# Optimization experiments

Hardware: AMD Instinct MI355X
Metric: run time of the kernel (lower is better)

## Reference

```python
import jax, jax.numpy as jnp
import numpy as np

N_NODES = 50000
N_EDGES = 800000
NODE_FEAT = 3
HID = 64
L = 4


def setup_inputs() -> dict:
    key = jax.random.key(0)
    ks = jax.random.split(key, 16)
    s = 0.05  # init scale
    inp = {
        'node_pos': jax.random.normal(ks[0], (N_NODES, 3), jnp.float32),
        'node_features': jax.random.normal(ks[1], (N_NODES, NODE_FEAT), jnp.float32),
        'edge_index': jax.random.randint(ks[2], (2, N_EDGES), 0, N_NODES, jnp.int64),
        # encoders
        'enc_w': jax.random.normal(ks[3], (NODE_FEAT, HID), jnp.float32) * s,
        'enc_b': jnp.zeros((HID,), jnp.float32),
        'edge_enc_w': jax.random.normal(ks[4], (3, HID), jnp.float32) * s,
        'edge_enc_b': jnp.zeros((HID,), jnp.float32),
        # stacked per-layer GNOLayer params
        'ew1': jax.random.normal(ks[5], (L, 3 * HID, HID), jnp.float32) * s,
        'eb1': jnp.zeros((L, HID), jnp.float32),
        'ew2': jax.random.normal(ks[6], (L, HID, HID), jnp.float32) * s,
        'eb2': jnp.zeros((L, HID), jnp.float32),
        'nw1': jax.random.normal(ks[7], (L, 2 * HID, HID), jnp.float32) * s,
        'nb1': jnp.zeros((L, HID), jnp.float32),
        'nw2': jax.random.normal(ks[8], (L, HID, HID), jnp.float32) * s,
        'nb2': jnp.zeros((L, HID), jnp.float32),
        # decoder
        'dec_w': jax.random.normal(ks[9], (HID, 1), jnp.float32) * s,
        'dec_b': jnp.zeros((1,), jnp.float32),
    }
    return inp


def reference(node_pos, node_features, edge_index, enc_w, enc_b, edge_enc_w,
              edge_enc_b, ew1, eb1, ew2, eb2, nw1, nb1, nw2, nb2, dec_w, dec_b):
    src, dst = edge_index[0], edge_index[1]
    edge_vec = node_pos[dst] - node_pos[src]            # [E, 3]
    h = node_features @ enc_w + enc_b                   # [N, H]
    e = edge_vec @ edge_enc_w + edge_enc_b              # [E, H]

    def layer(h, p):
        w1, b1, w2, b2, m1, c1, m2, c2 = p
        edge_in = jnp.concatenate([h[src], h[dst], e], axis=-1)   # [E, 3H]
        msg = jax.nn.relu(edge_in @ w1 + b1) @ w2 + b2            # [E, H]
        agg = jax.ops.segment_sum(msg, dst, num_segments=N_NODES)  # [N, H]
        node_in = jnp.concatenate([h, agg], axis=-1)              # [N, 2H]
        return jax.nn.relu(node_in @ m1 + c1) @ m2 + c2, None

    h, _ = jax.lax.scan(layer, h, (ew1, eb1, ew2, eb2, nw1, nb1, nw2, nb2))
    return h @ dec_w + dec_b                            # [N, 1]
```

## Files before the change

kernel.cpp:

```cpp
#include <hip/hip_runtime.h>

#define N_NODES 50000
#define N_EDGES 800000
#define HID 64
#define LAYERS 4
#define EP_CAP 2048
#define SCAN_NBLK 25

typedef unsigned short u16;
typedef __attribute__((ext_vector_type(8))) __bf16 bf16x8;
typedef __attribute__((ext_vector_type(8))) unsigned short u16x8;
typedef __attribute__((ext_vector_type(4))) float f32x4;
typedef _Float16 f16x2 __attribute__((ext_vector_type(2)));

__device__ __forceinline__ u16 f2bf(float f) {
  unsigned u = __builtin_bit_cast(unsigned, f);
  u += 0x7fffu + ((u >> 16) & 1u);
  return (u16)(u >> 16);
}
__device__ __forceinline__ float bf2f(u16 s) {
  return __builtin_bit_cast(float, ((unsigned)s) << 16);
}
__device__ __forceinline__ u16 f2h(float f) {
  return __builtin_bit_cast(u16, (_Float16)f);
}
__device__ __forceinline__ unsigned pkadd(unsigned a, unsigned b) {
  f16x2 r = __builtin_bit_cast(f16x2, a) + __builtin_bit_cast(f16x2, b);
  return __builtin_bit_cast(unsigned, r);
}
__device__ __forceinline__ unsigned pkmax0(unsigned x) {
  unsigned r, z = 0u;
  asm("v_pk_max_f16 %0, %1, %2" : "=v"(r) : "v"(x), "v"(z));
  return r;
}

__global__ __launch_bounds__(256) void init_kernel(
    const float* __restrict__ ew1, const float* __restrict__ eb1,
    const float* __restrict__ ew2, const float* __restrict__ eb2,
    const float* __restrict__ nw1, const float* __restrict__ nw2,
    const float* __restrict__ edge_enc_w, const float* __restrict__ edge_enc_b,
    u16* W1abT, float* Wvx, float* b1x,
    u16* NB1T, float* bb2, u16* M2T, int* __restrict__ cnt) {
  const int T = gridDim.x * 256;
  int tid = blockIdx.x * 256 + threadIdx.x;
  for (int i = tid; i < N_NODES; i += T) cnt[i] = 0;
  const int szA = LAYERS * 128 * 64, szV = LAYERS * 3 * 64, szB = LAYERS * 64;
  const int szN = LAYERS * 64 * 128, szb2 = LAYERS * 64, szM = LAYERS * 64 * 64;
  const int tot = szA + szV + szB + szN + szb2 + szM;
  for (int i = tid; i < tot; i += T) {
    int idx = i;
    if (idx < szA) {
      int l = idx / (128 * 64); int r = idx % (128 * 64);
      int nfc = r / 64; int k = r % 64;
      int half = nfc >> 6, f = nfc & 63;
      W1abT[idx] = f2bf(ew1[(l * 192 + half * 64 + k) * 64 + f]);
      continue;
    }
    idx -= szA;
    if (idx < szV) {
      int l = idx / 192, r = idx % 192, a = r / 64, f = r % 64;
      float s = 0.f;
      for (int m = 0; m < 64; ++m) s += edge_enc_w[a * 64 + m] * ew1[(l * 192 + 128 + m) * 64 + f];
      Wvx[idx] = s;
      continue;
    }
    idx -= szV;
    if (idx < szB) {
      int l = idx / 64, f = idx % 64;
      float s = eb1[l * 64 + f];
      for (int m = 0; m < 64; ++m) s += edge_enc_b[m] * ew1[(l * 192 + 128 + m) * 64 + f];
      b1x[idx] = s;
      continue;
    }
    idx -= szB;
    if (idx < szN) {
      int l = idx / 8192, r = idx % 8192, f = r / 128, k = r % 128;
      float v;
      if (k < 64) v = nw1[(l * 128 + k) * 64 + f];
      else {
        int j = k - 64; float s = 0.f;
        for (int g = 0; g < 64; ++g)
          s += ew2[(l * 64 + j) * 64 + g] * nw1[(l * 128 + 64 + g) * 64 + f];
        v = s;
      }
      NB1T[idx] = f2bf(v);
      continue;
    }
    idx -= szN;
    if (idx < szb2) {
      int l = idx / 64, f = idx % 64;
      float s = 0.f;
      for (int g = 0; g < 64; ++g) s += eb2[l * 64 + g] * nw1[(l * 128 + 64 + g) * 64 + f];
      bb2[idx] = s;
      continue;
    }
    idx -= szb2;
    int l = idx / 4096, r = idx % 4096, f = r / 64, k = r % 64;
    M2T[idx] = f2bf(nw2[(l * 64 + k) * 64 + f]);
  }
}

__global__ __launch_bounds__(256) void hist_kernel(const int* __restrict__ dstA,
                                                   int* __restrict__ cnt,
                                                   int* __restrict__ rank) {
  int idx = blockIdx.x * 256 + threadIdx.x;
  if (idx < N_EDGES) rank[idx] = atomicAdd(&cnt[dstA[idx]], 1);
}

__global__ __launch_bounds__(256) void scan1_kernel(const int* __restrict__ cnt,
                                                    int* __restrict__ offs,
                                                    int* __restrict__ partials) {
  __shared__ int sm[2048];
  __shared__ int ws2[256];
  int t = threadIdx.x, b = blockIdx.x;
  int base = b * 2048;
#pragma unroll
  for (int i = 0; i < 8; ++i) {
    int idx = base + i * 256 + t;
    sm[i * 256 + t] = (idx < N_NODES) ? cnt[idx] : 0;
  }
  __syncthreads();
  int loc[8]; int s = 0;
#pragma unroll
  for (int i = 0; i < 8; ++i) { loc[i] = s; s += sm[t * 8 + i]; }
  ws2[t] = s;
  __syncthreads();
  for (int off = 1; off < 256; off <<= 1) {
    int u = (t >= off) ? ws2[t - off] : 0;
    __syncthreads();
    ws2[t] += u;
    __syncthreads();
  }
  int tbase = (t > 0) ? ws2[t - 1] : 0;
  if (t == 255) partials[b] = ws2[255];
#pragma unroll
  for (int i = 0; i < 8; ++i) {
    int idx = base + t * 8 + i;
    if (idx < N_NODES) offs[idx] = tbase + loc[i];
  }
}

__global__ __launch_bounds__(256) void scan3_kernel(int* __restrict__ offs,
                                                    const int* __restrict__ partials) {
  __shared__ int pref;
  int blk = (blockIdx.x * 256) >> 11;
  if (threadIdx.x == 0) {
    int s = 0;
    for (int i = 0; i < blk; ++i) s += partials[i];
    pref = s;
  }
  __syncthreads();
  int idx = blockIdx.x * 256 + threadIdx.x;
  if (idx < N_NODES) offs[idx] += pref;
}

__global__ __launch_bounds__(256) void scatter_kernel(const int* __restrict__ ei,
                                                      const int* __restrict__ offs,
                                                      const int* __restrict__ rank,
                                                      int* __restrict__ srcB) {
  int idx = blockIdx.x * 256 + threadIdx.x;
  if (idx >= N_EDGES) return;
  int s = ei[idx], d = ei[N_EDGES + idx];
  srcB[offs[d] + rank[idx]] = s << 7;
}

__global__ __launch_bounds__(256) void encsu_kernel(
    const float* __restrict__ nf, const float* __restrict__ enc_w,
    const float* __restrict__ enc_b,
    const u16* __restrict__ W1abT, const float* __restrict__ Wvx,
    const float* __restrict__ b1x, const float* __restrict__ pos,
    u16* __restrict__ h, u16* __restrict__ Sarr, u16* __restrict__ Uarr) {
  __shared__ u16 hT[64 * 72];
  __shared__ float sPos[192];
  __shared__ float sNf[192];
  int t = threadIdx.x;
  int lane = t & 63, wvi = t >> 6;
  int n16 = lane & 15, quad = lane >> 4;
  int n0 = blockIdx.x * 64;
  if (t < 192) {
    int idx = n0 * 3 + t;
    bool ok = idx < N_NODES * 3;
    sPos[t] = ok ? pos[idx] : 0.f;
    sNf[t] = ok ? nf[idx] : 0.f;
  }
  __syncthreads();
  {
    int n = t >> 2, g = t & 3;
    float x0 = sNf[n * 3], x1 = sNf[n * 3 + 1], x2 = sNf[n * 3 + 2];
    u16x8 v0, v1;
#pragma unroll
    for (int j = 0; j < 8; ++j) {
      int jj = g * 16 + j;
      v0[j] = f2bf(enc_b[jj] + x0 * enc_w[jj] + x1 * enc_w[64 + jj] + x2 * enc_w[128 + jj]);
      int jj2 = jj + 8;
      v1[j] = f2bf(enc_b[jj2] + x0 * enc_w[jj2] + x1 * enc_w[64 + jj2] + x2 * enc_w[128 + jj2]);
    }
    *(u16x8*)(hT + n * 72 + g * 16) = v0;
    *(u16x8*)(hT + n * 72 + g * 16 + 8) = v1;
    int gn = n0 + n;
    if (gn < N_NODES) {
      *(u16x8*)(h + (size_t)gn * 64 + g * 16) = v0;
      *(u16x8*)(h + (size_t)gn * 64 + g * 16 + 8) = v1;
    }
  }
  __syncthreads();

  bf16x8 B[2][2];
  float w0[2], w1[2], w2[2], bb[2]; bool isU[2];
#pragma unroll
  for (int nt = 0; nt < 2; ++nt) {
    int col = wvi * 32 + nt * 16 + n16;
    const u16* p = W1abT + (size_t)col * 64 + quad * 8;
    B[nt][0] = __builtin_bit_cast(bf16x8, *(const u16x8*)(p));
    B[nt][1] = __builtin_bit_cast(bf16x8, *(const u16x8*)(p + 32));
    int f = col & 63; isU[nt] = col >= 64;
    w0[nt] = Wvx[f];
    w1[nt] = Wvx[64 + f];
    w2[nt] = Wvx[128 + f];
    bb[nt] = b1x[f];
  }
  f32x4 acc[4][2];
#pragma unroll
  for (int m = 0; m < 4; ++m)
#pragma unroll
    for (int nt = 0; nt < 2; ++nt) acc[m][nt] = (f32x4){0.f, 0.f, 0.f, 0.f};
#pragma unroll
  for (int m = 0; m < 4; ++m) {
    const u16* hp = hT + (m * 16 + n16) * 72 + quad * 8;
    bf16x8 a0 = __builtin_bit_cast(bf16x8, *(const u16x8*)(hp));
    bf16x8 a1 = __builtin_bit_cast(bf16x8, *(const u16x8*)(hp + 32));
#pragma unroll
    for (int nt = 0; nt < 2; ++nt) {
      acc[m][nt] = __builtin_amdgcn_mfma_f32_16x16x32_bf16(a0, B[nt][0], acc[m][nt], 0, 0, 0);
      acc[m][nt] = __builtin_amdgcn_mfma_f32_16x16x32_bf16(a1, B[nt][1], acc[m][nt], 0, 0, 0);
    }
  }
#pragma unroll
  for (int m = 0; m < 4; ++m)
#pragma unroll
    for (int nt = 0; nt < 2; ++nt) {
      int col = wvi * 32 + nt * 16 + n16;
      int f = col & 63;
#pragma unroll
      for (int r = 0; r < 4; ++r) {
        int e = m * 16 + quad * 4 + r;
        int grow = n0 + e;
        if (grow < N_NODES) {
          float P = sPos[e * 3] * w0[nt] + sPos[e * 3 + 1] * w1[nt] + sPos[e * 3 + 2] * w2[nt];
          if (!isU[nt]) Sarr[(size_t)grow * 64 + f] = f2h(acc[m][nt][r] - P);
          else          Uarr[(size_t)grow * 64 + f] = f2h(acc[m][nt][r] + P + bb[nt]);
        }
      }
    }
}

__global__ __launch_bounds__(256) void layer_kernel(
    const u16* __restrict__ h, const int* __restrict__ srcB,
    const int* __restrict__ offs,
    const u16* __restrict__ Sr, const u16* __restrict__ Ur,
    const u16* __restrict__ NB1T, const float* __restrict__ nb1,
    const float* __restrict__ bb2,
    const u16* __restrict__ M2T, const float* __restrict__ nb2,
    u16* __restrict__ hnext, int layer,
    const u16* __restrict__ W1abT, const float* __restrict__ Wvx,
    const float* __restrict__ b1x, const float* __restrict__ pos,
    u16* __restrict__ Sw, u16* __restrict__ Uw,
    const float* __restrict__ dec_w, const float* __restrict__ dec_b,
    float* __restrict__ out) {
  __shared__ int sIdx[EP_CAP];
  __shared__ int sOff[33];
  __shared__ u16 aggT[32 * 72];
  __shared__ u16 Hs[32 * 72];
  __shared__ float sPos[96];
  __shared__ float sRed[32][8];
  int t = threadIdx.x;
  int lane = t & 63, wvi = t >> 6;
  int n16 = lane & 15, quad = lane >> 4;
  int F = wvi * 16;
  int n0 = blockIdx.x * 32;

  if (t <= 32) {
    int d = n0 + t;
    sOff[t] = (d < N_NODES) ? offs[d] : N_EDGES;
  }
  if (t >= 64 && t < 160) {
    int i = t - 64;
    int idx = n0 * 3 + i;
    sPos[i] = (idx < N_NODES * 3) ? pos[idx] : 0.f;
  }
  __syncthreads();
  int eS = sOff[0];
  int nE = sOff[32] - eS;
  bool fit = (nE <= EP_CAP);
  if (fit) {
    for (int i = t; i < nE; i += 256) sIdx[i] = srcB[eS + i];
    if (t == 0 && nE < EP_CAP) sIdx[nE] = 0;
  }
  __syncthreads();

  {
    int c = lane & 31, half = lane >> 5;
    unsigned cbu = (unsigned)(c << 2);
    const char* __restrict__ Sb = (const char*)Sr;
    const char* __restrict__ Ub = (const char*)Ur;
    for (int i = 0; i < 8; i += 2) {
      int lnA = wvi * 8 + i;
      int dA = n0 + lnA;
      int e0A = sOff[lnA], degA = sOff[lnA + 1] - e0A;
      int e0B = sOff[lnA + 1], degB = sOff[lnA + 2] - e0B;
      int dAc = dA < N_NODES ? dA : N_NODES - 1;
      int dBc = (dA + 1) < N_NODES ? (dA + 1) : N_NODES - 1;
      unsigned upA = *(const unsigned*)(Ub + (size_t)dAc * 128 + cbu);
      unsigned upB = *(const unsigned*)(Ub + (size_t)dBc * 128 + cbu);
      float saA = 0.f, sbA = 0.f, saB = 0.f, sbB = 0.f;
      int relA = (degA > 0) ? (e0A - eS) : 0;
      int relB = (degB > 0) ? (e0B - eS) : 0;
      int g0A = (degA > 0) ? e0A : 0;
      int g0B = (degB > 0) ? e0B : 0;
      int degMin = degA < degB ? degA : degB;
      int degMax = degA > degB ? degA : degB;
      int fullr = degMin >> 4;
      int rmax = (degMax + 15) >> 4;
      if (fit) {
        int r = 0;
        for (; r < fullr; ++r) {
          int base = r * 16 + half;
          unsigned wA[8], wB[8];
#pragma unroll
          for (int kk = 0; kk < 8; ++kk) {
            int j = base + 2 * kk;
            wA[kk] = *(const unsigned*)(Sb + (unsigned)sIdx[relA + j] + cbu);
            wB[kk] = *(const unsigned*)(Sb + (unsigned)sIdx[relB + j] + cbu);
          }
          unsigned pA = 0u, pB = 0u;
#pragma unroll
          for (int kk = 0; kk < 8; ++kk) {
            pA = pkadd(pA, pkmax0(pkadd(wA[kk], upA)));
            pB = pkadd(pB, pkmax0(pkadd(wB[kk], upB)));
          }
          f16x2 hA2 = __builtin_bit_cast(f16x2, pA);
          f16x2 hB2 = __builtin_bit_cast(f16x2, pB);
          saA += (float)hA2[0]; sbA += (float)hA2[1];
          saB += (float)hB2[0]; sbB += (float)hB2[1];
        }
        for (; r < rmax; ++r) {
          int base = r * 16 + half;
          unsigned wA[8], wB[8]; bool okA[8], okB[8];
#pragma unroll
          for (int kk = 0; kk < 8; ++kk) {
            int j = base + 2 * kk;
            okA[kk] = j < degA;
            wA[kk] = *(const unsigned*)(Sb + (unsigned)sIdx[relA + (okA[kk] ? j : 0)] + cbu);
            okB[kk] = j < degB;
            wB[kk] = *(const unsigned*)(Sb + (unsigned)sIdx[relB + (okB[kk] ? j : 0)] + cbu);
          }
          unsigned pA = 0u, pB = 0u;
#pragma unroll
          for (int kk = 0; kk < 8; ++kk) {
            unsigned zA = pkmax0(pkadd(wA[kk], upA));
            pA = pkadd(pA, okA[kk] ? zA : 0u);
            unsigned zB = pkmax0(pkadd(wB[kk], upB));
            pB = pkadd(pB, okB[kk] ? zB : 0u);
          }
          f16x2 hA2 = __builtin_bit_cast(f16x2, pA);
          f16x2 hB2 = __builtin_bit_cast(f16x2, pB);
          saA += (float)hA2[0]; sbA += (float)hA2[1];
          saB += (float)hB2[0]; sbB += (float)hB2[1];
        }
      } else {
        for (int r = 0; r < rmax; ++r) {
          int base = r * 16 + half;
          unsigned wA[8], wB[8]; bool okA[8], okB[8];
#pragma unroll
          for (int kk = 0; kk < 8; ++kk) {
            int j = base + 2 * kk;
            okA[kk] = j < degA;
            wA[kk] = *(const unsigned*)(Sb + (unsigned)srcB[g0A + (okA[kk] ? j : 0)] + cbu);
            okB[kk] = j < degB;
            wB[kk] = *(const unsigned*)(Sb + (unsigned)srcB[g0B + (okB[kk] ? j : 0)] + cbu);
          }
          unsigned pA = 0u, pB = 0u;
#pragma unroll
          for (int kk = 0; kk < 8; ++kk) {
            unsigned zA = pkmax0(pkadd(wA[kk], upA));
            pA = pkadd(pA, okA[kk] ? zA : 0u);
            unsigned zB = pkmax0(pkadd(wB[kk], upB));
            pB = pkadd(pB, okB[kk] ? zB : 0u);
          }
          f16x2 hA2 = __builtin_bit_cast(f16x2, pA);
          f16x2 hB2 = __builtin_bit_cast(f16x2, pB);
          saA += (float)hA2[0]; sbA += (float)hA2[1];
          saB += (float)hB2[0]; sbB += (float)hB2[1];
        }
      }
      saA += __shfl_xor(saA, 32);  sbA += __shfl_xor(sbA, 32);
      saB += __shfl_xor(saB, 32);  sbB += __shfl_xor(sbB, 32);
      if (half == 0) {
        unsigned pk = (unsigned)f2bf(saA) | ((unsigned)f2bf(sbA) << 16);
        *(unsigned*)((char*)aggT + (size_t)lnA * 144 + cbu) = pk;
        unsigned pk2 = (unsigned)f2bf(saB) | ((unsigned)f2bf(sbB) << 16);
        *(unsigned*)((char*)aggT + (size_t)(lnA + 1) * 144 + cbu) = pk2;
      }
    }
  }
  __syncthreads();

  bf16x8 B1[4], B2[2];
  {
    const u16* p = NB1T + (size_t)(layer * 64 + F + n16) * 128 + quad * 8;
#pragma unroll
    for (int ks = 0; ks < 4; ++ks) B1[ks] = __builtin_bit_cast(bf16x8, *(const u16x8*)(p + ks * 32));
    const u16* q = M2T + (size_t)(layer * 64 + F + n16) * 64 + quad * 8;
#pragma unroll
    for (int ks = 0; ks < 2; ++ks) B2[ks] = __builtin_bit_cast(bf16x8, *(const u16x8*)(q + ks * 32));
  }
  float bias1 = nb1[layer * 64 + F + n16];
  float bb2f = bb2[layer * 64 + F + n16];
  float bias2 = nb2[layer * 64 + F + n16];

  f32x4 acc[2];
#pragma unroll
  for (int m = 0; m < 2; ++m) acc[m] = (f32x4){0.f, 0.f, 0.f, 0.f};
#pragma unroll
  for (int m = 0; m < 2; ++m) {
    int row = n0 + m * 16 + n16;
    if (row >= N_NODES) row = N_NODES - 1;
    const u16* hp = h + (size_t)row * 64 + quad * 8;
    const u16* ap = aggT + (m * 16 + n16) * 72 + quad * 8;
    bf16x8 a0 = __builtin_bit_cast(bf16x8, *(const u16x8*)(hp));
    bf16x8 a1 = __builtin_bit_cast(bf16x8, *(const u16x8*)(hp + 32));
    bf16x8 a2 = __builtin_bit_cast(bf16x8, *(const u16x8*)(ap));
    bf16x8 a3 = __builtin_bit_cast(bf16x8, *(const u16x8*)(ap + 32));
    acc[m] = __builtin_amdgcn_mfma_f32_16x16x32_bf16(a0, B1[0], acc[m], 0, 0, 0);
    acc[m] = __builtin_amdgcn_mfma_f32_16x16x32_bf16(a1, B1[1], acc[m], 0, 0, 0);
    acc[m] = __builtin_amdgcn_mfma_f32_16x16x32_bf16(a2, B1[2], acc[m], 0, 0, 0);
    acc[m] = __builtin_amdgcn_mfma_f32_16x16x32_bf16(a3, B1[3], acc[m], 0, 0, 0);
  }
#pragma unroll
  for (int m = 0; m < 2; ++m)
#pragma unroll
    for (int r = 0; r < 4; ++r) {
      int e = m * 16 + quad * 4 + r;
      float dg = (float)(sOff[e + 1] - sOff[e]);
      float v = acc[m][r] + bias1 + dg * bb2f;
      v = v > 0.f ? v : 0.f;
      Hs[e * 72 + F + n16] = f2bf(v);
    }
  __syncthreads();

  float c2[2][4];
#pragma unroll
  for (int m = 0; m < 2; ++m) {
    const u16* hp = Hs + (m * 16 + n16) * 72 + quad * 8;
    f32x4 cc = (f32x4){0.f, 0.f, 0.f, 0.f};
#pragma unroll
    for (int ks = 0; ks < 2; ++ks) {
      bf16x8 a = __builtin_bit_cast(bf16x8, *(const u16x8*)(hp + ks * 32));
      cc = __builtin_amdgcn_mfma_f32_16x16x32_bf16(a, B2[ks], cc, 0, 0, 0);
    }
#pragma unroll
    for (int r = 0; r < 4; ++r) c2[m][r] = cc[r] + bias2;
  }
  __syncthreads();

#pragma unroll
  for (int m = 0; m < 2; ++m)
#pragma unroll
    for (int r = 0; r < 4; ++r) {
      int e = m * 16 + quad * 4 + r;
      u16 hv = f2bf(c2[m][r]);
      Hs[e * 72 + F + n16] = hv;
      int gn = n0 + e;
      if (layer < LAYERS - 1 && gn < N_NODES)
        hnext[(size_t)gn * 64 + F + n16] = hv;
    }
  __syncthreads();

  if (layer < LAYERS - 1) {
    int lp = layer + 1;
    bf16x8 B3[2][2];
    float w0[2], w1[2], w2[2], bb[2]; bool isU[2];
#pragma unroll
    for (int nt = 0; nt < 2; ++nt) {
      int col = wvi * 32 + nt * 16 + n16;
      const u16* p = W1abT + (size_t)(lp * 128 + col) * 64 + quad * 8;
      B3[nt][0] = __builtin_bit_cast(bf16x8, *(const u16x8*)(p));
      B3[nt][1] = __builtin_bit_cast(bf16x8, *(const u16x8*)(p + 32));
      int f = col & 63; isU[nt] = col >= 64;
      w0[nt] = Wvx[(lp * 3 + 0) * 64 + f];
      w1[nt] = Wvx[(lp * 3 + 1) * 64 + f];
      w2[nt] = Wvx[(lp * 3 + 2) * 64 + f];
      bb[nt] = b1x[lp * 64 + f];
    }
    f32x4 a3[2][2];
#pragma unroll
    for (int m = 0; m < 2; ++m)
#pragma unroll
      for (int nt = 0; nt < 2; ++nt) a3[m][nt] = (f32x4){0.f, 0.f, 0.f, 0.f};
#pragma unroll
    for (int m = 0; m < 2; ++m) {
      const u16* hp = Hs + (m * 16 + n16) * 72 + quad * 8;
      bf16x8 a0 = __builtin_bit_cast(bf16x8, *(const u16x8*)(hp));
      bf16x8 a1 = __builtin_bit_cast(bf16x8, *(const u16x8*)(hp + 32));
#pragma unroll
      for (int nt = 0; nt < 2; ++nt) {
        a3[m][nt] = __builtin_amdgcn_mfma_f32_16x16x32_bf16(a0, B3[nt][0], a3[m][nt], 0, 0, 0);
        a3[m][nt] = __builtin_amdgcn_mfma_f32_16x16x32_bf16(a1, B3[nt][1], a3[m][nt], 0, 0, 0);
      }
    }
#pragma unroll
    for (int m = 0; m < 2; ++m)
#pragma unroll
      for (int nt = 0; nt < 2; ++nt) {
        int col = wvi * 32 + nt * 16 + n16;
        int f = col & 63;
#pragma unroll
        for (int r = 0; r < 4; ++r) {
          int e = m * 16 + quad * 4 + r;
          int grow = n0 + e;
          if (grow < N_NODES) {
            float P = sPos[e * 3] * w0[nt] + sPos[e * 3 + 1] * w1[nt] + sPos[e * 3 + 2] * w2[nt];
            if (!isU[nt]) Sw[(size_t)grow * 64 + f] = f2h(a3[m][nt][r] - P);
            else          Uw[(size_t)grow * 64 + f] = f2h(a3[m][nt][r] + P + bb[nt]);
          }
        }
      }
  } else {
    int e = t >> 3, part = t & 7;
    float s = 0.f;
#pragma unroll
    for (int j = 0; j < 8; ++j)
      s += bf2f(Hs[e * 72 + part * 8 + j]) * dec_w[part * 8 + j];
    sRed[e][part] = s;
    __syncthreads();
    if (part == 0) {
      int gn = n0 + e;
      if (gn < N_NODES) {
        float acc8 = dec_b[0];
#pragma unroll
        for (int p2 = 0; p2 < 8; ++p2) acc8 += sRed[e][p2];
        out[gn] = acc8;
      }
    }
  }
}

extern "C" void kernel_launch(void* const* d_in, const int* in_sizes, int n_in,
                              void* d_out, int out_size, void* d_ws, size_t ws_size,
                              hipStream_t stream) {
  const float* node_pos   = (const float*)d_in[0];
  const float* node_feat  = (const float*)d_in[1];
  const int*   edge_index = (const int*)d_in[2];
  const float* enc_w      = (const float*)d_in[3];
  const float* enc_b      = (const float*)d_in[4];
  const float* edge_enc_w = (const float*)d_in[5];
  const float* edge_enc_b = (const float*)d_in[6];
  const float* ew1        = (const float*)d_in[7];
  const float* eb1        = (const float*)d_in[8];
  const float* ew2        = (const float*)d_in[9];
  const float* eb2        = (const float*)d_in[10];
  const float* nw1        = (const float*)d_in[11];
  const float* nb1        = (const float*)d_in[12];
  const float* nw2        = (const float*)d_in[13];
  const float* nb2        = (const float*)d_in[14];
  const float* dec_w      = (const float*)d_in[15];
  const float* dec_b      = (const float*)d_in[16];
  float* out = (float*)d_out;

  char* ws = (char*)d_ws;
  size_t off = 0;
  u16*    hA    = (u16*)(ws + off);    off += (size_t)N_NODES * 64 * 2;
  u16*    hB    = (u16*)(ws + off);    off += (size_t)N_NODES * 64 * 2;
  u16*    S0    = (u16*)(ws + off);    off += (size_t)N_NODES * 64 * 2;
  u16*    U0    = (u16*)(ws + off);    off += (size_t)N_NODES * 64 * 2;
  u16*    S1    = (u16*)(ws + off);    off += (size_t)N_NODES * 64 * 2;
  u16*    U1    = (u16*)(ws + off);    off += (size_t)N_NODES * 64 * 2;
  u16*    W1abT = (u16*)(ws + off);    off += (size_t)LAYERS * 128 * 64 * 2;
  float*  Wvx   = (float*)(ws + off);  off += (size_t)LAYERS * 3 * 64 * 4;
  float*  b1x   = (float*)(ws + off);  off += (size_t)LAYERS * 64 * 4;
  u16*    NB1T  = (u16*)(ws + off);    off += (size_t)LAYERS * 64 * 128 * 2;
  float*  bb2   = (float*)(ws + off);  off += (size_t)LAYERS * 64 * 4;
  u16*    M2T   = (u16*)(ws + off);    off += (size_t)LAYERS * 64 * 64 * 2;
  int*    cnt      = (int*)(ws + off); off += (size_t)N_NODES * 4;
  int*    offsB    = (int*)(ws + off); off += (size_t)N_NODES * 4;
  int*    partials = (int*)(ws + off); off += 32 * 4;
  int*    rank     = (int*)(ws + off); off += (size_t)N_EDGES * 4;
  int*    srcB     = (int*)(ws + off); off += (size_t)N_EDGES * 4;

  const int* dstA = edge_index + N_EDGES;
  const int NBLK64 = (N_NODES + 63) / 64;
  const int NBLK32 = (N_NODES + 31) / 32;

  init_kernel<<<512, 256, 0, stream>>>(
      ew1, eb1, ew2, eb2, nw1, nw2, edge_enc_w, edge_enc_b,
      W1abT, Wvx, b1x, NB1T, bb2, M2T, cnt);

  hist_kernel<<<(N_EDGES + 255) / 256, 256, 0, stream>>>(dstA, cnt, rank);
  scan1_kernel<<<SCAN_NBLK, 256, 0, stream>>>(cnt, offsB, partials);
  scan3_kernel<<<(N_NODES + 255) / 256, 256, 0, stream>>>(offsB, partials);
  scatter_kernel<<<(N_EDGES + 255) / 256, 256, 0, stream>>>(edge_index, offsB, rank, srcB);

  encsu_kernel<<<NBLK64, 256, 0, stream>>>(node_feat, enc_w, enc_b,
                                           W1abT, Wvx, b1x, node_pos, hA, S0, U0);

  u16 *hc = hA, *hn = hB, *Sr = S0, *Ur = U0, *Sw = S1, *Uw = U1;
  for (int l = 0; l < LAYERS; ++l) {
    layer_kernel<<<NBLK32, 256, 0, stream>>>(hc, srcB, offsB, Sr, Ur,
                                             NB1T, nb1, bb2, M2T, nb2,
                                             hn, l, W1abT, Wvx, b1x, node_pos,
                                             Sw, Uw, dec_w, dec_b, out);
    u16* tmp;
    tmp = hc; hc = hn; hn = tmp;
    tmp = Sr; Sr = Sw; Sw = tmp;
    tmp = Ur; Ur = Uw; Uw = tmp;
  }
}
```

Baseline: 312.0 us.

## Merge preprocessing kernels to cut launch count in CSR build and encoder

Combines weight folding, node encoding and the destination histogram into one grid-stride prep kernel, with the count array cleared by a memset. It also merges the scan fix-up, the edge scatter and the S/U projection into a single kernel that reads h from global memory instead of recomputing it. The aim is to remove several small kernel launches and their serialization gaps in the setup phase. The cost is heavier kernels with mixed work. The partial-sum prefix is now recomputed by every block, and an extra offsets buffer is needed.

```diff
diff --git a/kernel.cpp b/kernel.cpp
--- a/kernel.cpp
+++ b/kernel.cpp
@@ -6,6 +6,8 @@
 #define LAYERS 4
 #define EP_CAP 2048
 #define SCAN_NBLK 25
+#define NBLK64 782
+#define NBLK32 1563
 
 typedef unsigned short u16;
 typedef __attribute__((ext_vector_type(8))) __bf16 bf16x8;
@@ -34,77 +36,89 @@
   return r;
 }
 
-__global__ __launch_bounds__(256) void init_kernel(
+__global__ __launch_bounds__(256) void prep_kernel(
+    const float* __restrict__ nf, const float* __restrict__ enc_w,
+    const float* __restrict__ enc_b,
     const float* __restrict__ ew1, const float* __restrict__ eb1,
     const float* __restrict__ ew2, const float* __restrict__ eb2,
     const float* __restrict__ nw1, const float* __restrict__ nw2,
     const float* __restrict__ edge_enc_w, const float* __restrict__ edge_enc_b,
-    u16* W1abT, float* Wvx, float* b1x,
-    u16* NB1T, float* bb2, u16* M2T, int* __restrict__ cnt) {
+    const int* __restrict__ dstA,
+    u16* __restrict__ h, u16* W1abT, float* Wvx, float* b1x,
+    u16* NB1T, float* bb2, u16* M2T,
+    int* __restrict__ cnt, int* __restrict__ rank) {
   const int T = gridDim.x * 256;
   int tid = blockIdx.x * 256 + threadIdx.x;
-  for (int i = tid; i < N_NODES; i += T) cnt[i] = 0;
-  const int szA = LAYERS * 128 * 64, szV = LAYERS * 3 * 64, szB = LAYERS * 64;
-  const int szN = LAYERS * 64 * 128, szb2 = LAYERS * 64, szM = LAYERS * 64 * 64;
-  const int tot = szA + szV + szB + szN + szb2 + szM;
-  for (int i = tid; i < tot; i += T) {
-    int idx = i;
-    if (idx < szA) {
-      int l = idx / (128 * 64); int r = idx % (128 * 64);
-      int nfc = r / 64; int k = r % 64;
-      int half = nfc >> 6, f = nfc & 63;
-      W1abT[idx] = f2bf(ew1[(l * 192 + half * 64 + k) * 64 + f]);
-      continue;
-    }
-    idx -= szA;
-    if (idx < szV) {
-      int l = idx / 192, r = idx % 192, a = r / 64, f = r % 64;
-      float s = 0.f;
-      for (int m = 0; m < 64; ++m) s += edge_enc_w[a * 64 + m] * ew1[(l * 192 + 128 + m) * 64 + f];
-      Wvx[idx] = s;
-      continue;
-    }
-    idx -= szV;
-    if (idx < szB) {
-      int l = idx / 64, f = idx % 64;
-      float s = eb1[l * 64 + f];
-      for (int m = 0; m < 64; ++m) s += edge_enc_b[m] * ew1[(l * 192 + 128 + m) * 64 + f];
-      b1x[idx] = s;
-      continue;
-    }
-    idx -= szB;
-    if (idx < szN) {
-      int l = idx / 8192, r = idx % 8192, f = r / 128, k = r % 128;
-      float v;
-      if (k < 64) v = nw1[(l * 128 + k) * 64 + f];
-      else {
-        int j = k - 64; float s = 0.f;
-        for (int g = 0; g < 64; ++g)
-          s += ew2[(l * 64 + j) * 64 + g] * nw1[(l * 128 + 64 + g) * 64 + f];
-        v = s;
-      }
-      NB1T[idx] = f2bf(v);
-      continue;
-    }
-    idx -= szN;
-    if (idx < szb2) {
-      int l = idx / 64, f = idx % 64;
-      float s = 0.f;
-      for (int g = 0; g < 64; ++g) s += eb2[l * 64 + g] * nw1[(l * 128 + 64 + g) * 64 + f];
-      bb2[idx] = s;
-      continue;
-    }
-    idx -= szb2;
-    int l = idx / 4096, r = idx % 4096, f = r / 64, k = r % 64;
-    M2T[idx] = f2bf(nw2[(l * 64 + k) * 64 + f]);
-  }
-}
-
-__global__ __launch_bounds__(256) void hist_kernel(const int* __restrict__ dstA,
-                                                   int* __restrict__ cnt,
-                                                   int* __restrict__ rank) {
-  int idx = blockIdx.x * 256 + threadIdx.x;
-  if (idx < N_EDGES) rank[idx] = atomicAdd(&cnt[dstA[idx]], 1);
+  {
+    const int szA = LAYERS * 128 * 64, szV = LAYERS * 3 * 64, szB = LAYERS * 64;
+    const int szN = LAYERS * 64 * 128, szb2 = LAYERS * 64, szM = LAYERS * 64 * 64;
+    const int tot = szA + szV + szB + szN + szb2 + szM;
+    for (int i = tid; i < tot; i += T) {
+      int idx = i;
+      if (idx < szA) {
+        int l = idx / (128 * 64); int r = idx % (128 * 64);
+        int nfc = r / 64; int k = r % 64;
+        int half = nfc >> 6, f = nfc & 63;
+        W1abT[idx] = f2bf(ew1[(l * 192 + half * 64 + k) * 64 + f]);
+        continue;
+      }
+      idx -= szA;
+      if (idx < szV) {
+        int l = idx / 192, r = idx % 192, a = r / 64, f = r % 64;
+        float s = 0.f;
+        for (int m = 0; m < 64; ++m) s += edge_enc_w[a * 64 + m] * ew1[(l * 192 + 128 + m) * 64 + f];
+        Wvx[idx] = s;
+        continue;
+      }
+      idx -= szV;
+      if (idx < szB) {
+        int l = idx / 64, f = idx % 64;
+        float s = eb1[l * 64 + f];
+        for (int m = 0; m < 64; ++m) s += edge_enc_b[m] * ew1[(l * 192 + 128 + m) * 64 + f];
+        b1x[idx] = s;
+        continue;
+      }
+      idx -= szB;
+      if (idx < szN) {
+        int l = idx / 8192, r = idx % 8192, f = r / 128, k = r % 128;
+        float v;
+        if (k < 64) v = nw1[(l * 128 + k) * 64 + f];
+        else {
+          int j = k - 64; float s = 0.f;
+          for (int g = 0; g < 64; ++g)
+            s += ew2[(l * 64 + j) * 64 + g] * nw1[(l * 128 + 64 + g) * 64 + f];
+          v = s;
+        }
+        NB1T[idx] = f2bf(v);
+        continue;
+      }
+      idx -= szN;
+      if (idx < szb2) {
+        int l = idx / 64, f = idx % 64;
+        float s = 0.f;
+        for (int g = 0; g < 64; ++g) s += eb2[l * 64 + g] * nw1[(l * 128 + 64 + g) * 64 + f];
+        bb2[idx] = s;
+        continue;
+      }
+      idx -= szb2;
+      int l = idx / 4096, r = idx % 4096, f = r / 64, k = r % 64;
+      M2T[idx] = f2bf(nw2[(l * 64 + k) * 64 + f]);
+    }
+  }
+  for (int i = tid; i < N_NODES * 8; i += T) {
+    int n = i >> 3, j0 = (i & 7) * 8;
+    float x0 = nf[n * 3 + 0], x1 = nf[n * 3 + 1], x2 = nf[n * 3 + 2];
+    u16x8 v;
+#pragma unroll
+    for (int j = 0; j < 8; ++j) {
+      int jj = j0 + j;
+      float s = enc_b[jj] + x0 * enc_w[jj] + x1 * enc_w[64 + jj] + x2 * enc_w[128 + jj];
+      v[j] = f2bf(s);
+    }
+    *(u16x8*)(h + (size_t)n * 64 + j0) = v;
+  }
+  for (int idx = tid; idx < N_EDGES; idx += T)
+    rank[idx] = atomicAdd(&cnt[dstA[idx]], 1);
 }
 
 __global__ __launch_bounds__(256) void scan1_kernel(const int* __restrict__ cnt,
@@ -140,118 +154,94 @@
   }
 }
 
-__global__ __launch_bounds__(256) void scan3_kernel(int* __restrict__ offs,
-                                                    const int* __restrict__ partials) {
-  __shared__ int pref;
-  int blk = (blockIdx.x * 256) >> 11;
-  if (threadIdx.x == 0) {
-    int s = 0;
-    for (int i = 0; i < blk; ++i) s += partials[i];
-    pref = s;
-  }
-  __syncthreads();
-  int idx = blockIdx.x * 256 + threadIdx.x;
-  if (idx < N_NODES) offs[idx] += pref;
-}
-
-__global__ __launch_bounds__(256) void scatter_kernel(const int* __restrict__ ei,
-                                                      const int* __restrict__ offs,
-                                                      const int* __restrict__ rank,
-                                                      int* __restrict__ srcB) {
-  int idx = blockIdx.x * 256 + threadIdx.x;
-  if (idx >= N_EDGES) return;
-  int s = ei[idx], d = ei[N_EDGES + idx];
-  srcB[offs[d] + rank[idx]] = s << 7;
-}
-
-__global__ __launch_bounds__(256) void encsu_kernel(
-    const float* __restrict__ nf, const float* __restrict__ enc_w,
-    const float* __restrict__ enc_b,
-    const u16* __restrict__ W1abT, const float* __restrict__ Wvx,
-    const float* __restrict__ b1x, const float* __restrict__ pos,
-    u16* __restrict__ h, u16* __restrict__ Sarr, u16* __restrict__ Uarr) {
-  __shared__ u16 hT[64 * 72];
+__global__ __launch_bounds__(256) void fss_kernel(
+    const u16* __restrict__ h, const u16* __restrict__ W1abT,
+    const float* __restrict__ Wvx, const float* __restrict__ b1x,
+    const float* __restrict__ pos,
+    u16* __restrict__ Sarr, u16* __restrict__ Uarr,
+    const int* __restrict__ offs, const int* __restrict__ partials,
+    const int* __restrict__ ei, const int* __restrict__ rank,
+    int* __restrict__ srcB, int* __restrict__ offs2) {
   __shared__ float sPos[192];
-  __shared__ float sNf[192];
-  int t = threadIdx.x;
-  int lane = t & 63, wvi = t >> 6;
-  int n16 = lane & 15, quad = lane >> 4;
-  int n0 = blockIdx.x * 64;
-  if (t < 192) {
-    int idx = n0 * 3 + t;
-    bool ok = idx < N_NODES * 3;
-    sPos[t] = ok ? pos[idx] : 0.f;
-    sNf[t] = ok ? nf[idx] : 0.f;
-  }
-  __syncthreads();
-  {
-    int n = t >> 2, g = t & 3;
-    float x0 = sNf[n * 3], x1 = sNf[n * 3 + 1], x2 = sNf[n * 3 + 2];
-    u16x8 v0, v1;
-#pragma unroll
-    for (int j = 0; j < 8; ++j) {
-      int jj = g * 16 + j;
-      v0[j] = f2bf(enc_b[jj] + x0 * enc_w[jj] + x1 * enc_w[64 + jj] + x2 * enc_w[128 + jj]);
-      int jj2 = jj + 8;
-      v1[j] = f2bf(enc_b[jj2] + x0 * enc_w[jj2] + x1 * enc_w[64 + jj2] + x2 * enc_w[128 + jj2]);
-    }
-    *(u16x8*)(hT + n * 72 + g * 16) = v0;
-    *(u16x8*)(hT + n * 72 + g * 16 + 8) = v1;
-    int gn = n0 + n;
-    if (gn < N_NODES) {
-      *(u16x8*)(h + (size_t)gn * 64 + g * 16) = v0;
-      *(u16x8*)(h + (size_t)gn * 64 + g * 16 + 8) = v1;
-    }
-  }
-  __syncthreads();
-
-  bf16x8 B[2][2];
-  float w0[2], w1[2], w2[2], bb[2]; bool isU[2];
-#pragma unroll
-  for (int nt = 0; nt < 2; ++nt) {
-    int col = wvi * 32 + nt * 16 + n16;
-    const u16* p = W1abT + (size_t)col * 64 + quad * 8;
-    B[nt][0] = __builtin_bit_cast(bf16x8, *(const u16x8*)(p));
-    B[nt][1] = __builtin_bit_cast(bf16x8, *(const u16x8*)(p + 32));
-    int f = col & 63; isU[nt] = col >= 64;
-    w0[nt] = Wvx[f];
-    w1[nt] = Wvx[64 + f];
-    w2[nt] = Wvx[128 + f];
-    bb[nt] = b1x[f];
-  }
-  f32x4 acc[4][2];
-#pragma unroll
-  for (int m = 0; m < 4; ++m)
-#pragma unroll
-    for (int nt = 0; nt < 2; ++nt) acc[m][nt] = (f32x4){0.f, 0.f, 0.f, 0.f};
-#pragma unroll
-  for (int m = 0; m < 4; ++m) {
-    const u16* hp = hT + (m * 16 + n16) * 72 + quad * 8;
-    bf16x8 a0 = __builtin_bit_cast(bf16x8, *(const u16x8*)(hp));
-    bf16x8 a1 = __builtin_bit_cast(bf16x8, *(const u16x8*)(hp + 32));
-#pragma unroll
-    for (int nt = 0; nt < 2; ++nt) {
-      acc[m][nt] = __builtin_amdgcn_mfma_f32_16x16x32_bf16(a0, B[nt][0], acc[m][nt], 0, 0, 0);
-      acc[m][nt] = __builtin_amdgcn_mfma_f32_16x16x32_bf16(a1, B[nt][1], acc[m][nt], 0, 0, 0);
-    }
-  }
-#pragma unroll
-  for (int m = 0; m < 4; ++m)
+  __shared__ int psum[32];
+  int t = threadIdx.x, b = blockIdx.x;
+
+  if (b < NBLK64) {
+    int lane = t & 63, wvi = t >> 6;
+    int n16 = lane & 15, quad = lane >> 4;
+    int n0 = b * 64;
+    if (t < 192) {
+      int idx = n0 * 3 + t;
+      sPos[t] = (idx < N_NODES * 3) ? pos[idx] : 0.f;
+    }
+    __syncthreads();
+
+    bf16x8 B[2][2];
+    float w0[2], w1[2], w2[2], bb[2]; bool isU[2];
 #pragma unroll
     for (int nt = 0; nt < 2; ++nt) {
       int col = wvi * 32 + nt * 16 + n16;
-      int f = col & 63;
-#pragma unroll
-      for (int r = 0; r < 4; ++r) {
-        int e = m * 16 + quad * 4 + r;
-        int grow = n0 + e;
-        if (grow < N_NODES) {
-          float P = sPos[e * 3] * w0[nt] + sPos[e * 3 + 1] * w1[nt] + sPos[e * 3 + 2] * w2[nt];
-          if (!isU[nt]) Sarr[(size_t)grow * 64 + f] = f2h(acc[m][nt][r] - P);
-          else          Uarr[(size_t)grow * 64 + f] = f2h(acc[m][nt][r] + P + bb[nt]);
+      const u16* p = W1abT + (size_t)col * 64 + quad * 8;
+      B[nt][0] = __builtin_bit_cast(bf16x8, *(const u16x8*)(p));
+      B[nt][1] = __builtin_bit_cast(bf16x8, *(const u16x8*)(p + 32));
+      int f = col & 63; isU[nt] = col >= 64;
+      w0[nt] = Wvx[f];
+      w1[nt] = Wvx[64 + f];
+      w2[nt] = Wvx[128 + f];
+      bb[nt] = b1x[f];
+    }
+    f32x4 acc[4][2];
+#pragma unroll
+    for (int m = 0; m < 4; ++m)
+#pragma unroll
+      for (int nt = 0; nt < 2; ++nt) acc[m][nt] = (f32x4){0.f, 0.f, 0.f, 0.f};
+#pragma unroll
+    for (int m = 0; m < 4; ++m) {
+      int row = n0 + m * 16 + n16;
+      if (row >= N_NODES) row = N_NODES - 1;
+      const u16* hp = h + (size_t)row * 64 + quad * 8;
+      bf16x8 a0 = __builtin_bit_cast(bf16x8, *(const u16x8*)(hp));
+      bf16x8 a1 = __builtin_bit_cast(bf16x8, *(const u16x8*)(hp + 32));
+#pragma unroll
+      for (int nt = 0; nt < 2; ++nt) {
+        acc[m][nt] = __builtin_amdgcn_mfma_f32_16x16x32_bf16(a0, B[nt][0], acc[m][nt], 0, 0, 0);
+        acc[m][nt] = __builtin_amdgcn_mfma_f32_16x16x32_bf16(a1, B[nt][1], acc[m][nt], 0, 0, 0);
+      }
+    }
+#pragma unroll
+    for (int m = 0; m < 4; ++m)
+#pragma unroll
+      for (int nt = 0; nt < 2; ++nt) {
+        int col = wvi * 32 + nt * 16 + n16;
+        int f = col & 63;
+#pragma unroll
+        for (int r = 0; r < 4; ++r) {
+          int e = m * 16 + quad * 4 + r;
+          int grow = n0 + e;
+          if (grow < N_NODES) {
+            float P = sPos[e * 3] * w0[nt] + sPos[e * 3 + 1] * w1[nt] + sPos[e * 3 + 2] * w2[nt];
+            if (!isU[nt]) Sarr[(size_t)grow * 64 + f] = f2h(acc[m][nt][r] - P);
+            else          Uarr[(size_t)grow * 64 + f] = f2h(acc[m][nt][r] + P + bb[nt]);
+          }
         }
       }
-    }
+  }
+
+  if (t == 0) {
+    int s = 0;
+#pragma unroll
+    for (int i = 0; i < SCAN_NBLK; ++i) { psum[i] = s; s += partials[i]; }
+  }
+  __syncthreads();
+
+  int tid = b * 256 + t;
+  const int T = gridDim.x * 256;
+  for (int idx = tid; idx < N_NODES; idx += T)
+    offs2[idx] = offs[idx] + psum[idx >> 11];
+  for (int idx = tid; idx < N_EDGES; idx += T) {
+    int s = ei[idx], d = ei[N_EDGES + idx];
+    srcB[offs[d] + psum[d >> 11] + rank[idx]] = s << 7;
+  }
 }
 
 __global__ __launch_bounds__(256) void layer_kernel(
@@ -582,26 +572,26 @@
   float*  bb2   = (float*)(ws + off);  off += (size_t)LAYERS * 64 * 4;
   u16*    M2T   = (u16*)(ws + off);    off += (size_t)LAYERS * 64 * 64 * 2;
   int*    cnt      = (int*)(ws + off); off += (size_t)N_NODES * 4;
+  int*    offsA    = (int*)(ws + off); off += (size_t)N_NODES * 4;
   int*    offsB    = (int*)(ws + off); off += (size_t)N_NODES * 4;
   int*    partials = (int*)(ws + off); off += 32 * 4;
   int*    rank     = (int*)(ws + off); off += (size_t)N_EDGES * 4;
   int*    srcB     = (int*)(ws + off); off += (size_t)N_EDGES * 4;
 
   const int* dstA = edge_index + N_EDGES;
-  const int NBLK64 = (N_NODES + 63) / 64;
-  const int NBLK32 = (N_NODES + 31) / 32;
-
-  init_kernel<<<512, 256, 0, stream>>>(
-      ew1, eb1, ew2, eb2, nw1, nw2, edge_enc_w, edge_enc_b,
-      W1abT, Wvx, b1x, NB1T, bb2, M2T, cnt);
-
-  hist_kernel<<<(N_EDGES + 255) / 256, 256, 0, stream>>>(dstA, cnt, rank);
-  scan1_kernel<<<SCAN_NBLK, 256, 0, stream>>>(cnt, offsB, partials);
-  scan3_kernel<<<(N_NODES + 255) / 256, 256, 0, stream>>>(offsB, partials);
-  scatter_kernel<<<(N_EDGES + 255) / 256, 256, 0, stream>>>(edge_index, offsB, rank, srcB);
-
-  encsu_kernel<<<NBLK64, 256, 0, stream>>>(node_feat, enc_w, enc_b,
-                                           W1abT, Wvx, b1x, node_pos, hA, S0, U0);
+
+  hipMemsetAsync(cnt, 0, (size_t)N_NODES * 4, stream);
+
+  prep_kernel<<<3125, 256, 0, stream>>>(
+      node_feat, enc_w, enc_b, ew1, eb1, ew2, eb2, nw1, nw2,
+      edge_enc_w, edge_enc_b, dstA,
+      hA, W1abT, Wvx, b1x, NB1T, bb2, M2T, cnt, rank);
+
+  scan1_kernel<<<SCAN_NBLK, 256, 0, stream>>>(cnt, offsA, partials);
+
+  fss_kernel<<<NBLK32, 256, 0, stream>>>(
+      hA, W1abT, Wvx, b1x, node_pos, S0, U0,
+      offsA, partials, edge_index, rank, srcB, offsB);
 
   u16 *hc = hA, *hn = hB, *Sr = S0, *Ur = U0, *Sw = S1, *Uw = U1;
   for (int l = 0; l < LAYERS; ++l) {
```

Result: faster. 300.7 us (-3.6%).
